# Performance work log

Measured on AMD Instinct MI355X. Metric: run time of the kernel, lower is better.

Reference implementation:

```python
import jax, jax.numpy as jnp
import numpy as np

WIND_SIZE = 5
EPSILON = 1e-5
ALPHA = 1.0


def _windows(a, w):
    # a: [B,1,H,W] -> [B, w*w, H, W], zero-padded, window index in (di,dj) row-major
    # order matching torch's unfold(dim=2).unfold(dim=3) + reshape.
    p = w // 2
    B, _, H, W = a.shape
    ap = jnp.pad(a[:, 0], ((0, 0), (p, p), (p, p)))
    taps = [ap[:, i:i + H, j:j + W] for i in range(w) for j in range(w)]
    return jnp.stack(taps, axis=1)


def setup_inputs() -> dict:
    key = jax.random.key(0)
    ks = jax.random.split(key, 6)
    B, H, W = 4, 512, 512
    ww = WIND_SIZE * WIND_SIZE
    fake = jax.random.uniform(ks[0], (B, 1, H, W), dtype=jnp.float32)
    gamma_hdr = jax.random.uniform(ks[1], (B, 1, H, W), dtype=jnp.float32)
    # strictly positive so hdr**(1-f) is well defined
    hdr_original_im = jax.random.uniform(ks[2], (B, 1, H, W), dtype=jnp.float32) + 0.01
    r_weights = jax.random.uniform(ks[3], (B, ww, H, W), dtype=jnp.float32)
    # f_factors in [0.5, 1.5] to avoid division blow-up, realistic gamma factors
    f_factors = jax.random.uniform(ks[4], (B,), dtype=jnp.float32) + 0.5
    hdr_original_gray = jax.random.uniform(ks[5], (B, 1, H, W), dtype=jnp.float32)
    return {
        'fake': fake,
        'gamma_hdr': gamma_hdr,
        'hdr_original_im': hdr_original_im,
        'r_weights': r_weights,
        'f_factors': f_factors,
        'hdr_original_gray': hdr_original_gray,
    }


def reference(fake, gamma_hdr, hdr_original_im, r_weights, f_factors, hdr_original_gray):
    w = WIND_SIZE
    eps = jnp.float32(EPSILON)
    # create_window -> uniform window, normalized: every tap weight = 1/(w*w)
    dist_gauss = jnp.float32(1.0 / (w * w))
    weights_map = dist_gauss * r_weights                      # [B, w*w, H, W]
    weights_map_sum = jnp.sum(weights_map, axis=1, keepdims=True)  # [B,1,H,W]

    def bf_stats(x):
        xw = _windows(x, w)                                   # [B, w*w, H, W]
        mu = jnp.sum(xw * weights_map, axis=1, keepdims=True) / weights_map_sum
        var = jnp.sum((xw - mu) ** 2 * weights_map, axis=1, keepdims=True) / weights_map_sum
        std = jnp.sqrt(jnp.maximum(var, 0.0) + eps)
        return mu, std

    _, std_fake = bf_stats(fake)
    _, std_gamma = bf_stats(gamma_hdr)

    ff = f_factors[:, None, None, None]                       # [B,1,1,1]
    hdr_pow = jnp.power(hdr_original_im, 1.0 - ff)
    hw = _windows(hdr_pow, w)
    hdr_pow_mu = jnp.sum(hw * weights_map, axis=1, keepdims=True) / weights_map_sum

    w_blf = jnp.sum(r_weights, axis=1, keepdims=True) - 1.0   # [B,1,H,W]

    std_objective = (ALPHA / ff) * std_gamma * (hdr_pow_mu + eps)
    gray_max = jnp.max(hdr_original_gray.reshape(hdr_original_gray.shape[0], -1), axis=1)
    std_objective = std_objective * gray_max[:, None, None, None]

    res = 1.0 - std_fake / (std_fake + jax.lax.stop_gradient(std_objective))
    res = res * (w_blf / jnp.mean(w_blf))
    return jnp.mean(res)
```

## Files before the change

### kernel.cpp

```cpp
#include <hip/hip_runtime.h>

#define Bn 4
#define Hn 512
#define Wn 512
#define HWn (Hn * Wn)

constexpr float kEps = 1e-5f;


__global__ __launch_bounds__(256) void gmax_kernel(
    const float* __restrict__ gray, unsigned int* __restrict__ gmax_bits) {
  const int b = blockIdx.y;
  const int i = (blockIdx.x * 256 + threadIdx.x) << 2;
  const float4 g4 = *(const float4*)(gray + b * HWn + i);
  float lmax = fmaxf(fmaxf(g4.x, g4.y), fmaxf(g4.z, g4.w));
#pragma unroll
  for (int off = 32; off > 0; off >>= 1)
    lmax = fmaxf(lmax, __shfl_down(lmax, off));
  __shared__ float smax[4];
  const int lane = threadIdx.x & 63, wid = threadIdx.x >> 6;
  if (lane == 0) smax[wid] = lmax;
  __syncthreads();
  if (threadIdx.x == 0) {
    float m = fmaxf(fmaxf(smax[0], smax[1]), fmaxf(smax[2], smax[3]));
    atomicMax(&gmax_bits[b], __float_as_uint(m));
  }
}

__global__ __launch_bounds__(512, 4) void main_kernel(
    const float* __restrict__ fake, const float* __restrict__ gamma,
    const float* __restrict__ hdr, const float* __restrict__ rw,
    const float* __restrict__ ff, const unsigned int* __restrict__ gmax_bits,
    float* __restrict__ acc) {
  __shared__ float smem[3][8][512];
  __shared__ float sh1[8], sh2[8];

  const int b = blockIdx.x >> 7;
  const int h0 = (blockIdx.x & 127) << 2;
  const float e = 1.0f - ff[b];

  const float* fb = fake + (size_t)b * HWn;
  const float* gb = gamma + (size_t)b * HWn;
  const float* hb = hdr + (size_t)b * HWn;

  const int t = threadIdx.x;
  const int lr = t >> 7;
  const int w0 = (t & 127) << 2;
  const int h = h0 + lr;
  const float* rwb = rw + (size_t)b * 25 * HWn + (h << 9) + w0;

  float4 wv[5];
#pragma unroll
  for (int d = 0; d < 5; ++d)
    wv[d] = *(const float4*)(rwb + (size_t)d * HWn);

  float4* smem4 = (float4*)smem;
#pragma unroll
  for (int k = 0; k < 6; ++k) {
    const int i = t + (k << 9);
    const int a = i >> 10;
    const int rem = i & 1023;
    const int r = rem >> 7;
    const int c4 = rem & 127;
    const int grow = min(max(h0 - 2 + r, 0), Hn - 1);
    const float* src = (a == 0) ? fb : (a == 1) ? gb : hb;
    float4 v = *(const float4*)(src + (grow << 9) + (c4 << 2));
    if (a == 2) {
      v.x = __powf(v.x, e);
      v.y = __powf(v.y, e);
      v.z = __powf(v.z, e);
      v.w = __powf(v.w, e);
    }
    smem4[i] = v;
  }
  __syncthreads();

  float Sw[4] = {0, 0, 0, 0}, Sf[4] = {0, 0, 0, 0}, Sf2[4] = {0, 0, 0, 0};
  float Sg[4] = {0, 0, 0, 0}, Sg2[4] = {0, 0, 0, 0}, Sh[4] = {0, 0, 0, 0};

  float cm[12];
#pragma unroll
  for (int i = 2; i < 10; ++i)
    cm[i] = ((unsigned)(w0 - 4 + i) < (unsigned)Wn) ? 1.0f : 0.0f;
  const int c0 = max(w0 - 4, 0);
  const int c2 = min(w0 + 4, Wn - 4);

#pragma unroll
  for (int dyi = 0; dyi < 5; ++dyi) {
    const int r = lr + dyi;
    const float rmask = ((unsigned)(h + dyi - 2) < (unsigned)Hn) ? 1.0f : 0.0f;

    float4 wc[5];
#pragma unroll
    for (int d = 0; d < 5; ++d) wc[d] = wv[d];
    if (dyi < 4) {
#pragma unroll
      for (int d = 0; d < 5; ++d)
        wv[d] = *(const float4*)(rwb + (size_t)((dyi + 1) * 5 + d) * HWn);
    }

    const float4 f0 = *(const float4*)&smem[0][r][c0];
    const float4 f1 = *(const float4*)&smem[0][r][w0];
    const float4 f2 = *(const float4*)&smem[0][r][c2];
    const float4 g0 = *(const float4*)&smem[1][r][c0];
    const float4 g1 = *(const float4*)&smem[1][r][w0];
    const float4 g2 = *(const float4*)&smem[1][r][c2];
    const float4 p0 = *(const float4*)&smem[2][r][c0];
    const float4 p1 = *(const float4*)&smem[2][r][w0];
    const float4 p2 = *(const float4*)&smem[2][r][c2];

    float xf[12] = {f0.x, f0.y, f0.z, f0.w, f1.x, f1.y, f1.z, f1.w,
                    f2.x, f2.y, f2.z, f2.w};
    float xg[12] = {g0.x, g0.y, g0.z, g0.w, g1.x, g1.y, g1.z, g1.w,
                    g2.x, g2.y, g2.z, g2.w};
    float xh[12] = {p0.x, p0.y, p0.z, p0.w, p1.x, p1.y, p1.z, p1.w,
                    p2.x, p2.y, p2.z, p2.w};
#pragma unroll
    for (int i2 = 2; i2 < 10; ++i2) {
      const float m = rmask * cm[i2];
      xf[i2] *= m;
      xg[i2] *= m;
      xh[i2] *= m;
    }
#pragma unroll
    for (int dxi = 0; dxi < 5; ++dxi) {
      const float wk[4] = {wc[dxi].x, wc[dxi].y, wc[dxi].z, wc[dxi].w};
#pragma unroll
      for (int j = 0; j < 4; ++j) {
        const float w = wk[j];
        const float f = xf[j + dxi + 2], g = xg[j + dxi + 2],
                    hp = xh[j + dxi + 2];
        Sw[j] += w;
        Sf[j] = fmaf(w, f, Sf[j]);
        Sf2[j] = fmaf(w * f, f, Sf2[j]);
        Sg[j] = fmaf(w, g, Sg[j]);
        Sg2[j] = fmaf(w * g, g, Sg2[j]);
        Sh[j] = fmaf(w, hp, Sh[j]);
      }
    }
  }

  const float ffb = ff[b];
  const float gmax = __uint_as_float(gmax_bits[b]);
  float s1 = 0.0f, s2 = 0.0f;
#pragma unroll
  for (int j = 0; j < 4; ++j) {
    const float invSw = 1.0f / Sw[j];
    const float muf = Sf[j] * invSw;
    const float varf = fmaxf(Sf2[j] * invSw - muf * muf, 0.0f);
    const float stdf = sqrtf(varf + kEps);
    const float mug = Sg[j] * invSw;
    const float varg = fmaxf(Sg2[j] * invSw - mug * mug, 0.0f);
    const float stdg = sqrtf(varg + kEps);
    const float hpmu = Sh[j] * invSw;
    const float stdobj = (1.0f / ffb) * stdg * (hpmu + kEps) * gmax;
    const float r = 1.0f - stdf / (stdf + stdobj);
    const float wblf = Sw[j] - 1.0f;
    s1 = fmaf(r, wblf, s1);
    s2 += wblf;
  }
#pragma unroll
  for (int off = 32; off > 0; off >>= 1) {
    s1 += __shfl_down(s1, off);
    s2 += __shfl_down(s2, off);
  }
  const int lane = t & 63, wid = t >> 6;
  if (lane == 0) {
    sh1[wid] = s1;
    sh2[wid] = s2;
  }
  __syncthreads();
  if (t == 0) {
    float a1 = 0.0f, a2 = 0.0f;
#pragma unroll
    for (int i = 0; i < 8; ++i) {
      a1 += sh1[i];
      a2 += sh2[i];
    }
    atomicAdd(&acc[0], a1);
    atomicAdd(&acc[1], a2);
  }
}

__global__ void final_kernel(const float* __restrict__ acc,
                             float* __restrict__ out) {
  if (threadIdx.x == 0) out[0] = acc[0] / acc[1];
}

extern "C" void kernel_launch(void* const* d_in, const int* in_sizes, int n_in,
                              void* d_out, int out_size, void* d_ws,
                              size_t ws_size, hipStream_t stream) {
  const float* fake = (const float*)d_in[0];
  const float* gamma = (const float*)d_in[1];
  const float* hdr = (const float*)d_in[2];
  const float* rw = (const float*)d_in[3];
  const float* ff = (const float*)d_in[4];
  const float* gray = (const float*)d_in[5];
  float* out = (float*)d_out;
  float* ws = (float*)d_ws;
  unsigned int* gmax_bits = (unsigned int*)ws;
  float* acc = ws + 4;

  hipMemsetAsync(d_ws, 0, 64, stream);
  gmax_kernel<<<dim3(HWn / 1024, Bn), 256, 0, stream>>>(gray, gmax_bits);
  main_kernel<<<Bn * Hn / 4, 512, 0, stream>>>(fake, gamma, hdr, rw, ff,
                                               gmax_bits, acc);
  final_kernel<<<1, 64, 0, stream>>>(acc, out);
}
```

Before: 190.1 us.

## Double-buffer r_weights prefetch two rows ahead and fuse final division

The r_weights loads are now prefetched two window rows ahead into alternating register buffers, so more global loads are in flight during the accumulation. The separate final kernel is removed: the last block to finish, found through an atomic done counter, computes the output ratio. This saves one kernel launch but raises register pressure under launch_bounds(512,4), which could cause spills.

```diff
diff --git a/kernel.cpp b/kernel.cpp
--- a/kernel.cpp
+++ b/kernel.cpp
@@ -31,7 +31,8 @@
     const float* __restrict__ fake, const float* __restrict__ gamma,
     const float* __restrict__ hdr, const float* __restrict__ rw,
     const float* __restrict__ ff, const unsigned int* __restrict__ gmax_bits,
-    float* __restrict__ acc) {
+    float* __restrict__ acc, unsigned int* __restrict__ done,
+    float* __restrict__ out) {
   __shared__ float smem[3][8][512];
   __shared__ float sh1[8], sh2[8];
 
@@ -49,10 +50,13 @@
   const int h = h0 + lr;
   const float* rwb = rw + (size_t)b * 25 * HWn + (h << 9) + w0;
 
-  float4 wv[5];
+  float4 wA[5], wB[5];
 #pragma unroll
   for (int d = 0; d < 5; ++d)
-    wv[d] = *(const float4*)(rwb + (size_t)d * HWn);
+    wA[d] = *(const float4*)(rwb + (size_t)d * HWn);
+#pragma unroll
+  for (int d = 0; d < 5; ++d)
+    wB[d] = *(const float4*)(rwb + (size_t)(5 + d) * HWn);
 
   float4* smem4 = (float4*)smem;
 #pragma unroll
@@ -92,11 +96,17 @@
 
     float4 wc[5];
 #pragma unroll
-    for (int d = 0; d < 5; ++d) wc[d] = wv[d];
-    if (dyi < 4) {
-#pragma unroll
-      for (int d = 0; d < 5; ++d)
-        wv[d] = *(const float4*)(rwb + (size_t)((dyi + 1) * 5 + d) * HWn);
+    for (int d = 0; d < 5; ++d) wc[d] = (dyi & 1) ? wB[d] : wA[d];
+    if (dyi < 3) {
+#pragma unroll
+      for (int d = 0; d < 5; ++d) {
+        const float4 v =
+            *(const float4*)(rwb + (size_t)((dyi + 2) * 5 + d) * HWn);
+        if (dyi & 1)
+          wB[d] = v;
+        else
+          wA[d] = v;
+      }
     }
 
     const float4 f0 = *(const float4*)&smem[0][r][c0];
@@ -179,12 +189,14 @@
     }
     atomicAdd(&acc[0], a1);
     atomicAdd(&acc[1], a2);
-  }
-}
-
-__global__ void final_kernel(const float* __restrict__ acc,
-                             float* __restrict__ out) {
-  if (threadIdx.x == 0) out[0] = acc[0] / acc[1];
+    __threadfence();
+    const unsigned int old = atomicAdd(done, 1u);
+    if (old == (unsigned int)(gridDim.x - 1)) {
+      const float v0 = atomicAdd(&acc[0], 0.0f);
+      const float v1 = atomicAdd(&acc[1], 0.0f);
+      out[0] = v0 / v1;
+    }
+  }
 }
 
 extern "C" void kernel_launch(void* const* d_in, const int* in_sizes, int n_in,
@@ -200,10 +212,10 @@
   float* ws = (float*)d_ws;
   unsigned int* gmax_bits = (unsigned int*)ws;
   float* acc = ws + 4;
+  unsigned int* done = (unsigned int*)(ws + 6);
 
   hipMemsetAsync(d_ws, 0, 64, stream);
   gmax_kernel<<<dim3(HWn / 1024, Bn), 256, 0, stream>>>(gray, gmax_bits);
   main_kernel<<<Bn * Hn / 4, 512, 0, stream>>>(fake, gamma, hdr, rw, ff,
-                                               gmax_bits, acc);
-  final_kernel<<<1, 64, 0, stream>>>(acc, out);
+                                               gmax_bits, acc, done, out);
 }
```

Measured after the change: 210.6 us. 10.8% more time.
